# Kernel optimization log

Hardware: AMD Instinct MI355X
Metric: run time of the kernel (lower is better)

The kernel has to match this reference:

```python
import jax, jax.numpy as jnp
import numpy as np

EPS = 1e-08
LAMBDA_SIM = 1.0
LAMBDA_SPARSITY = 0.001
B, D, K = 8192, 4096, 64


def setup_inputs() -> dict:
    key = jax.random.key(0)
    k1, k2, k3, k4, k5 = jax.random.split(key, 5)
    labels = jax.random.randint(k1, (B,), 0, K)
    hard_class_probs = jax.nn.one_hot(labels, K, dtype=jnp.float32)  # [B,K] hard one-hot
    return {
        "hard_class_probs": hard_class_probs,
        "masked_activations_1b": jax.random.normal(k2, (B, D), dtype=jnp.float32),
        "masked_activations_8b": jax.random.normal(k3, (B, D), dtype=jnp.float32),
        "mask_1b": jax.random.uniform(k4, (B, D), dtype=jnp.float32),
        "mask_8b": jax.random.uniform(k5, (B, D), dtype=jnp.float32),
    }


def _classwise_pairwise_cossim(acts, hard_class_probs):
    # F.normalize(p=2, dim=-1, eps=EPS): x / max(||x||, eps)
    norms = jnp.sqrt(jnp.sum(acts * acts, axis=-1, keepdims=True))
    norm_acts = acts / jnp.maximum(norms, EPS)                      # [B,D]
    S = norm_acts @ norm_acts.T                                      # [B,B] gram of unit vectors
    diag = jnp.sum(norm_acts * norm_acts, axis=-1)                   # [B] (== diag(S))
    M = (hard_class_probs > 0.5).astype(acts.dtype)                  # [B,K] hard membership
    n = jnp.sum(M, axis=0)                                           # [K] class counts
    SM = S @ M                                                       # [B,K]
    mSm = jnp.sum(M * SM, axis=0)                                    # [K] sum_{i,j in class} S_ij
    sum_diag = M.T @ diag                                            # [K]
    pair_sum = 0.5 * (mSm - sum_diag)                                # sum over i<j pairs
    n_pairs = 0.5 * n * (n - 1.0)
    valid = n >= 2.0
    per_class_mean = jnp.where(valid, pair_sum / jnp.maximum(n_pairs, 1.0), 0.0)
    n_valid = jnp.sum(valid.astype(acts.dtype))
    return jnp.where(n_valid > 0, jnp.sum(per_class_mean) / jnp.maximum(n_valid, 1.0), 0.0)


def _binary_entropy(p):
    p = jnp.clip(p, EPS, 1.0 - EPS)
    return jnp.mean(-(p * jnp.log(p) + (1.0 - p) * jnp.log(1.0 - p)))


def _combined_loss(hard_class_probs, masked_activations, mask):
    sim_loss = -_classwise_pairwise_cossim(masked_activations, hard_class_probs)
    sparsity_loss = _binary_entropy(mask)
    total = LAMBDA_SIM * sim_loss + LAMBDA_SPARSITY * sparsity_loss
    return total, sim_loss, sparsity_loss


def reference(hard_class_probs, masked_activations_1b, masked_activations_8b, mask_1b, mask_8b):
    loss_1b, sim_1b, sp_1b = _combined_loss(hard_class_probs, masked_activations_1b, mask_1b)
    loss_8b, sim_8b, sp_8b = _combined_loss(hard_class_probs, masked_activations_8b, mask_8b)
    total_loss = loss_1b + loss_8b
    return (total_loss, sim_1b, sim_8b, sp_1b, sp_8b)
```

## Files before the change

kernel.cpp:

```cpp
#include <hip/hip_runtime.h>
#include <math.h>

#define B_ 8192
#define D_ 4096
#define K_ 64
#define EPSF 1e-8f
#define LN2F 0.69314718056f
#define SPLITS 16
#define ECHUNKS 1024

typedef float f32x4 __attribute__((ext_vector_type(4)));


__global__ void k_init(int* __restrict__ z) {
  if (threadIdx.x < 192) z[threadIdx.x] = 0;
}

__global__ void k_labels(const float* __restrict__ probs, int* __restrict__ counts,
                         int* __restrict__ rowlist) {
  int row = blockIdx.x * 4 + (threadIdx.x >> 6);
  int lane = threadIdx.x & 63;
  float p = probs[(size_t)row * K_ + lane];
  unsigned long long m = __ballot(p > 0.5f);
  if (lane == 0) {
    int k = __ffsll(m) - 1;
    if (k >= 0) {
      int pos = atomicAdd(&counts[k], 1);
      rowlist[k * B_ + pos] = row;
    }
  }
}

__device__ __forceinline__ float ent1(float p) {
  p = fminf(fmaxf(p, EPSF), 1.0f - EPSF);
  float q = 1.0f - p;
  float lp = __builtin_amdgcn_logf(p);
  float lq = __builtin_amdgcn_logf(fmaxf(q, 1e-38f));
  return -(p * lp + q * lq);
}

__device__ __forceinline__ float ent4(f32x4 v) {
  return ent1(v.x) + ent1(v.y) + ent1(v.z) + ent1(v.w);
}

__global__ __launch_bounds__(256) void k_fused(
    const float* __restrict__ a1, const float* __restrict__ a8,
    const f32x4* __restrict__ m1, const f32x4* __restrict__ m8,
    const int* __restrict__ counts, const int* __restrict__ rowlist,
    float* __restrict__ Cpart1, float* __restrict__ Cpart8, float* __restrict__ sd1,
    float* __restrict__ sd8, double* __restrict__ entpart) {
  __shared__ float sh[8];
  int t = threadIdx.x;
  if (blockIdx.x & 1) {
    int blk = blockIdx.x >> 1;
    const f32x4* base = ((blk < ECHUNKS) ? m1 : m8) + (size_t)(blk & (ECHUNKS - 1)) * 8192;
    double* ep = entpart + ((blk < ECHUNKS) ? 0 : ECHUNKS);
    float s = 0.f;
#pragma unroll
    for (int o = 0; o < 4; ++o) {
      f32x4 v[8];
#pragma unroll
      for (int j = 0; j < 8; ++j) v[j] = base[t + (o * 8 + j) * 256];
#pragma unroll
      for (int j = 0; j < 8; ++j) s += ent4(v[j]);
    }
#pragma unroll
    for (int o = 32; o > 0; o >>= 1) s += __shfl_down(s, o);
    if ((t & 63) == 0) sh[t >> 6] = s;
    __syncthreads();
    if (t == 0) ep[blk & (ECHUNKS - 1)] = (double)((sh[0] + sh[1] + sh[2] + sh[3]) * LN2F);
  } else {
    int bid2 = blockIdx.x >> 1;
    const float* a = (bid2 < 1024) ? a1 : a8;
    float* Cpart = (bid2 < 1024) ? Cpart1 : Cpart8;
    float* sd = (bid2 < 1024) ? sd1 : sd8;
    int b2 = bid2 & 1023;
    int k = b2 & 63;
    int split = b2 >> 6;
    int wave = t >> 6;
    int lane = t & 63;
    int cnt = counts[k];
    int beg = (cnt * split) / SPLITS;
    int end = (cnt * (split + 1)) / SPLITS;
    const int* rl = rowlist + k * B_;

    f32x4 acc0 = 0.f, acc1 = 0.f, acc2 = 0.f, acc3 = 0.f;
    float sdacc = 0.f;
    int par = 0;
    for (int r = beg; r < end; ++r, par ^= 1) {
      int row = rl[r];
      const f32x4* rp = (const f32x4*)(a + (size_t)row * D_) + (wave * 256 + lane);
      f32x4 v0 = rp[0];
      f32x4 v1 = rp[64];
      f32x4 v2 = rp[128];
      f32x4 v3 = rp[192];
      float s = v0.x * v0.x + v0.y * v0.y + v0.z * v0.z + v0.w * v0.w;
      s += v1.x * v1.x + v1.y * v1.y + v1.z * v1.z + v1.w * v1.w;
      s += v2.x * v2.x + v2.y * v2.y + v2.z * v2.z + v2.w * v2.w;
      s += v3.x * v3.x + v3.y * v3.y + v3.z * v3.z + v3.w * v3.w;
#pragma unroll
      for (int o = 32; o > 0; o >>= 1) s += __shfl_xor(s, o);
      if (lane == 0) sh[par * 4 + wave] = s;
      __syncthreads();
      float stot = sh[par * 4] + sh[par * 4 + 1] + sh[par * 4 + 2] + sh[par * 4 + 3];
      float w = 1.0f / fmaxf(sqrtf(stot), EPSF);
      acc0 += w * v0;
      acc1 += w * v1;
      acc2 += w * v2;
      acc3 += w * v3;
      sdacc += stot * w * w;
    }

    float* cp = Cpart + ((size_t)split * K_ + k) * D_ + wave * 1024;
    *(f32x4*)(cp + 4 * lane) = acc0;
    *(f32x4*)(cp + 4 * (64 + lane)) = acc1;
    *(f32x4*)(cp + 4 * (128 + lane)) = acc2;
    *(f32x4*)(cp + 4 * (192 + lane)) = acc3;
    if (t == 0 && sdacc != 0.f) atomicAdd(&sd[k], sdacc);
  }
}

__global__ __launch_bounds__(256) void k_msm(const float* __restrict__ Cpart1,
                                             const float* __restrict__ Cpart8,
                                             float* __restrict__ msp1,
                                             float* __restrict__ msp8) {
  __shared__ float lds[4];
  int b = blockIdx.x;
  const float* Cpart = (b < 256) ? Cpart1 : Cpart8;
  float* msp = (b < 256) ? msp1 : msp8;
  b &= 255;
  int k = b >> 2;
  int q = b & 3;
  int t = threadIdx.x;
  int col = q * 1024 + 4 * t;
  f32x4 c = 0.f;
#pragma unroll
  for (int s = 0; s < SPLITS; ++s)
    c += *(const f32x4*)(Cpart + ((size_t)s * K_ + k) * D_ + col);
  float sq = c.x * c.x + c.y * c.y + c.z * c.z + c.w * c.w;
#pragma unroll
  for (int o = 32; o > 0; o >>= 1) sq += __shfl_down(sq, o);
  if ((t & 63) == 0) lds[t >> 6] = sq;
  __syncthreads();
  if (t == 0) msp[blockIdx.x & 255] = lds[0] + lds[1] + lds[2] + lds[3];
}

__global__ void k_final(const double* __restrict__ entpart, const int* __restrict__ counts,
                        const float* __restrict__ sd1, const float* __restrict__ sd8,
                        const float* __restrict__ msp1, const float* __restrict__ msp8,
                        float* __restrict__ out) {
  __shared__ double dl[8];
  int t = threadIdx.x;
  double e1 = 0.0, e8 = 0.0;
  for (int i = t; i < ECHUNKS; i += 256) {
    e1 += entpart[i];
    e8 += entpart[ECHUNKS + i];
  }
#pragma unroll
  for (int o = 32; o > 0; o >>= 1) {
    e1 += __shfl_down(e1, o);
    e8 += __shfl_down(e8, o);
  }
  int wid = t >> 6;
  if ((t & 63) == 0) { dl[wid] = e1; dl[4 + wid] = e8; }
  __syncthreads();
  float pcm1 = 0.f, pcm8 = 0.f, valid = 0.f;
  if (t < K_) {
    float mSm1 = msp1[t * 4] + msp1[t * 4 + 1] + msp1[t * 4 + 2] + msp1[t * 4 + 3];
    float mSm8 = msp8[t * 4] + msp8[t * 4 + 1] + msp8[t * 4 + 2] + msp8[t * 4 + 3];
    float n = (float)counts[t];
    bool v = (n >= 2.0f);
    float np = fmaxf(0.5f * n * (n - 1.0f), 1.0f);
    valid = v ? 1.0f : 0.f;
    pcm1 = v ? 0.5f * (mSm1 - sd1[t]) / np : 0.f;
    pcm8 = v ? 0.5f * (mSm8 - sd8[t]) / np : 0.f;
  }
#pragma unroll
  for (int o = 32; o > 0; o >>= 1) {
    pcm1 += __shfl_down(pcm1, o);
    pcm8 += __shfl_down(pcm8, o);
    valid += __shfl_down(valid, o);
  }
  if (t == 0) {
    double etot1 = dl[0] + dl[1] + dl[2] + dl[3];
    double etot8 = dl[4] + dl[5] + dl[6] + dl[7];
    float sp1 = (float)(etot1 / (double)((long long)B_ * D_));
    float sp8 = (float)(etot8 / (double)((long long)B_ * D_));
    float cs1 = (valid > 0.f) ? pcm1 / fmaxf(valid, 1.0f) : 0.f;
    float cs8 = (valid > 0.f) ? pcm8 / fmaxf(valid, 1.0f) : 0.f;
    float sim1 = -cs1, sim8 = -cs8;
    out[0] = sim1 + sim8 + 0.001f * (sp1 + sp8);
    out[1] = sim1;
    out[2] = sim8;
    out[3] = sp1;
    out[4] = sp8;
  }
}


extern "C" void kernel_launch(void* const* d_in, const int* in_sizes, int n_in,
                              void* d_out, int out_size, void* d_ws, size_t ws_size,
                              hipStream_t stream) {
  const float* probs = (const float*)d_in[0];
  const float* a1 = (const float*)d_in[1];
  const float* a8 = (const float*)d_in[2];
  const float* m1 = (const float*)d_in[3];
  const float* m8 = (const float*)d_in[4];
  float* out = (float*)d_out;
  char* ws = (char*)d_ws;

  double* entpart = (double*)(ws + 0);
  int* counts = (int*)(ws + 16384);
  float* sd1 = (float*)(ws + 16640);
  float* sd8 = (float*)(ws + 16896);
  float* msp1 = (float*)(ws + 17152);
  float* msp8 = (float*)(ws + 18176);
  int* rowlist = (int*)(ws + 32768);
  float* Cpart1 = (float*)(ws + 2129920);
  float* Cpart8 = (float*)(ws + 18907136);

  k_init<<<1, 256, 0, stream>>>(counts);
  k_labels<<<B_ / 4, 256, 0, stream>>>(probs, counts, rowlist);
  k_fused<<<4096, 256, 0, stream>>>(a1, a8, (const f32x4*)m1, (const f32x4*)m8, counts,
                                    rowlist, Cpart1, Cpart8, sd1, sd8, entpart);
  k_msm<<<512, 256, 0, stream>>>(Cpart1, Cpart8, msp1, msp8);
  k_final<<<1, 256, 0, stream>>>(entpart, counts, sd1, sd8, msp1, msp8, out);
}
```

Measured before the change: 169.6 us.

## Interleave entropy mask chunks into class-sum blocks within one loop

Before, even and odd blocks did different jobs: odd blocks computed mask entropy and even blocks did the per-class normalized row sums. Now each block does both, mixing its 8 entropy iterations of 4 loads each into the row-sum loop. The grid is halved to 2048 blocks. The aim is to overlap the mask-entropy loads with the latency-bound row-gather loop and cut the number of blocks, at the cost of more registers per thread and an extra barrier and reduction at the end of each block.

```diff
diff --git a/kernel.cpp b/kernel.cpp
--- a/kernel.cpp
+++ b/kernel.cpp
@@ -7,7 +7,7 @@
 #define EPSF 1e-8f
 #define LN2F 0.69314718056f
 #define SPLITS 16
-#define ECHUNKS 1024
+#define ECH 1024
 
 typedef float f32x4 __attribute__((ext_vector_type(4)));
 
@@ -50,50 +50,51 @@
     float* __restrict__ Cpart1, float* __restrict__ Cpart8, float* __restrict__ sd1,
     float* __restrict__ sd8, double* __restrict__ entpart) {
   __shared__ float sh[8];
+  int b = blockIdx.x;
+  int tensor = b >> 10;
+  int g = b & 1023;
+  const float* a = tensor ? a8 : a1;
+  const f32x4* mask = tensor ? m8 : m1;
+  float* Cpart = tensor ? Cpart8 : Cpart1;
+  float* sd = tensor ? sd8 : sd1;
+  double* ep = entpart + tensor * ECH;
+  int k = g & 63;
+  int split = g >> 6;
   int t = threadIdx.x;
-  if (blockIdx.x & 1) {
-    int blk = blockIdx.x >> 1;
-    const f32x4* base = ((blk < ECHUNKS) ? m1 : m8) + (size_t)(blk & (ECHUNKS - 1)) * 8192;
-    double* ep = entpart + ((blk < ECHUNKS) ? 0 : ECHUNKS);
-    float s = 0.f;
-#pragma unroll
-    for (int o = 0; o < 4; ++o) {
-      f32x4 v[8];
-#pragma unroll
-      for (int j = 0; j < 8; ++j) v[j] = base[t + (o * 8 + j) * 256];
-#pragma unroll
-      for (int j = 0; j < 8; ++j) s += ent4(v[j]);
-    }
-#pragma unroll
-    for (int o = 32; o > 0; o >>= 1) s += __shfl_down(s, o);
-    if ((t & 63) == 0) sh[t >> 6] = s;
-    __syncthreads();
-    if (t == 0) ep[blk & (ECHUNKS - 1)] = (double)((sh[0] + sh[1] + sh[2] + sh[3]) * LN2F);
-  } else {
-    int bid2 = blockIdx.x >> 1;
-    const float* a = (bid2 < 1024) ? a1 : a8;
-    float* Cpart = (bid2 < 1024) ? Cpart1 : Cpart8;
-    float* sd = (bid2 < 1024) ? sd1 : sd8;
-    int b2 = bid2 & 1023;
-    int k = b2 & 63;
-    int split = b2 >> 6;
-    int wave = t >> 6;
-    int lane = t & 63;
-    int cnt = counts[k];
-    int beg = (cnt * split) / SPLITS;
-    int end = (cnt * (split + 1)) / SPLITS;
-    const int* rl = rowlist + k * B_;
-
-    f32x4 acc0 = 0.f, acc1 = 0.f, acc2 = 0.f, acc3 = 0.f;
-    float sdacc = 0.f;
-    int par = 0;
-    for (int r = beg; r < end; ++r, par ^= 1) {
-      int row = rl[r];
+  int wave = t >> 6;
+  int lane = t & 63;
+  int cnt = counts[k];
+  int beg = (cnt * split) / SPLITS;
+  int end = (cnt * (split + 1)) / SPLITS;
+  const int* rl = rowlist + k * B_;
+  const f32x4* mbase = mask + (size_t)g * 8192;
+
+  f32x4 acc0 = 0.f, acc1 = 0.f, acc2 = 0.f, acc3 = 0.f;
+  float sdacc = 0.f, entacc = 0.f;
+  int nrows = end - beg;
+  int iters = (nrows > 8) ? nrows : 8;
+  int par = 0;
+  for (int i = 0; i < iters; ++i, par ^= 1) {
+    bool doEnt = (i < 8);
+    bool doRow = (i < nrows);
+    f32x4 e0, e1, e2, e3;
+    if (doEnt) {
+      e0 = mbase[t + (4 * i + 0) * 256];
+      e1 = mbase[t + (4 * i + 1) * 256];
+      e2 = mbase[t + (4 * i + 2) * 256];
+      e3 = mbase[t + (4 * i + 3) * 256];
+    }
+    f32x4 v0, v1, v2, v3;
+    if (doRow) {
+      int row = rl[beg + i];
       const f32x4* rp = (const f32x4*)(a + (size_t)row * D_) + (wave * 256 + lane);
-      f32x4 v0 = rp[0];
-      f32x4 v1 = rp[64];
-      f32x4 v2 = rp[128];
-      f32x4 v3 = rp[192];
+      v0 = rp[0];
+      v1 = rp[64];
+      v2 = rp[128];
+      v3 = rp[192];
+    }
+    if (doEnt) entacc += ent4(e0) + ent4(e1) + ent4(e2) + ent4(e3);
+    if (doRow) {
       float s = v0.x * v0.x + v0.y * v0.y + v0.z * v0.z + v0.w * v0.w;
       s += v1.x * v1.x + v1.y * v1.y + v1.z * v1.z + v1.w * v1.w;
       s += v2.x * v2.x + v2.y * v2.y + v2.z * v2.z + v2.w * v2.w;
@@ -108,16 +109,23 @@
       acc1 += w * v1;
       acc2 += w * v2;
       acc3 += w * v3;
-      sdacc += stot * w * w;
-    }
-
-    float* cp = Cpart + ((size_t)split * K_ + k) * D_ + wave * 1024;
-    *(f32x4*)(cp + 4 * lane) = acc0;
-    *(f32x4*)(cp + 4 * (64 + lane)) = acc1;
-    *(f32x4*)(cp + 4 * (128 + lane)) = acc2;
-    *(f32x4*)(cp + 4 * (192 + lane)) = acc3;
-    if (t == 0 && sdacc != 0.f) atomicAdd(&sd[k], sdacc);
-  }
+      if (t == 0) sdacc += stot * w * w;
+    }
+  }
+
+  float* cp = Cpart + ((size_t)split * K_ + k) * D_ + wave * 1024;
+  *(f32x4*)(cp + 4 * lane) = acc0;
+  *(f32x4*)(cp + 4 * (64 + lane)) = acc1;
+  *(f32x4*)(cp + 4 * (128 + lane)) = acc2;
+  *(f32x4*)(cp + 4 * (192 + lane)) = acc3;
+  if (t == 0 && sdacc != 0.f) atomicAdd(&sd[k], sdacc);
+
+  __syncthreads();
+#pragma unroll
+  for (int o = 32; o > 0; o >>= 1) entacc += __shfl_down(entacc, o);
+  if (lane == 0) sh[wave] = entacc;
+  __syncthreads();
+  if (t == 0) ep[g] = (double)((sh[0] + sh[1] + sh[2] + sh[3]) * LN2F);
 }
 
 __global__ __launch_bounds__(256) void k_msm(const float* __restrict__ Cpart1,
@@ -152,9 +160,9 @@
   __shared__ double dl[8];
   int t = threadIdx.x;
   double e1 = 0.0, e8 = 0.0;
-  for (int i = t; i < ECHUNKS; i += 256) {
+  for (int i = t; i < ECH; i += 256) {
     e1 += entpart[i];
-    e8 += entpart[ECHUNKS + i];
+    e8 += entpart[ECH + i];
   }
 #pragma unroll
   for (int o = 32; o > 0; o >>= 1) {
@@ -221,7 +229,7 @@
 
   k_init<<<1, 256, 0, stream>>>(counts);
   k_labels<<<B_ / 4, 256, 0, stream>>>(probs, counts, rowlist);
-  k_fused<<<4096, 256, 0, stream>>>(a1, a8, (const f32x4*)m1, (const f32x4*)m8, counts,
+  k_fused<<<2048, 256, 0, stream>>>(a1, a8, (const f32x4*)m1, (const f32x4*)m8, counts,
                                     rowlist, Cpart1, Cpart8, sd1, sd8, entpart);
   k_msm<<<512, 256, 0, stream>>>(Cpart1, Cpart8, msp1, msp8);
   k_final<<<1, 256, 0, stream>>>(entpart, counts, sd1, sd8, msp1, msp8, out);
```

After: 171.6 us. No clear change (+1.2%).

## Software-pipeline row loads and group fused-kernel blocks by type in chunks of eight

Applied to the files above, without the earlier changes.

The class-accumulation loop now double-buffers rows: it loads the next row's four vectors before reducing and normalising the current one, so global-load latency overlaps the barrier and reduction. Block-to-work mapping also changes from alternating odd/even blocks to groups of eight consecutive blocks per work type, which changes how entropy and accumulation blocks interleave across the GPU. The prefetch raises register pressure, and the loop body is duplicated through macros.

```diff
diff --git a/kernel.cpp b/kernel.cpp
--- a/kernel.cpp
+++ b/kernel.cpp
@@ -7,7 +7,7 @@
 #define EPSF 1e-8f
 #define LN2F 0.69314718056f
 #define SPLITS 16
-#define ECHUNKS 1024
+#define ECH 1024
 
 typedef float f32x4 __attribute__((ext_vector_type(4)));
 
@@ -50,17 +50,22 @@
     float* __restrict__ Cpart1, float* __restrict__ Cpart8, float* __restrict__ sd1,
     float* __restrict__ sd8, double* __restrict__ entpart) {
   __shared__ float sh[8];
+  int b = blockIdx.x;
+  int grp = b >> 3;
+  int lane8 = b & 7;
+  int type = grp & 1;
+  int id = (grp >> 1) * 8 + lane8;
   int t = threadIdx.x;
-  if (blockIdx.x & 1) {
-    int blk = blockIdx.x >> 1;
-    const f32x4* base = ((blk < ECHUNKS) ? m1 : m8) + (size_t)(blk & (ECHUNKS - 1)) * 8192;
-    double* ep = entpart + ((blk < ECHUNKS) ? 0 : ECHUNKS);
+
+  if (type) {
+    const f32x4* mbase = ((id >> 10) ? m8 : m1) + (size_t)(id & 1023) * 8192;
+    double* ep = entpart + ((id >> 10) ? ECH : 0);
     float s = 0.f;
 #pragma unroll
     for (int o = 0; o < 4; ++o) {
       f32x4 v[8];
 #pragma unroll
-      for (int j = 0; j < 8; ++j) v[j] = base[t + (o * 8 + j) * 256];
+      for (int j = 0; j < 8; ++j) v[j] = mbase[t + (o * 8 + j) * 256];
 #pragma unroll
       for (int j = 0; j < 8; ++j) s += ent4(v[j]);
     }
@@ -68,15 +73,14 @@
     for (int o = 32; o > 0; o >>= 1) s += __shfl_down(s, o);
     if ((t & 63) == 0) sh[t >> 6] = s;
     __syncthreads();
-    if (t == 0) ep[blk & (ECHUNKS - 1)] = (double)((sh[0] + sh[1] + sh[2] + sh[3]) * LN2F);
+    if (t == 0) ep[id & 1023] = (double)((sh[0] + sh[1] + sh[2] + sh[3]) * LN2F);
   } else {
-    int bid2 = blockIdx.x >> 1;
-    const float* a = (bid2 < 1024) ? a1 : a8;
-    float* Cpart = (bid2 < 1024) ? Cpart1 : Cpart8;
-    float* sd = (bid2 < 1024) ? sd1 : sd8;
-    int b2 = bid2 & 1023;
-    int k = b2 & 63;
-    int split = b2 >> 6;
+    int tensor = id >> 10;
+    const float* a = tensor ? a8 : a1;
+    float* Cpart = tensor ? Cpart8 : Cpart1;
+    float* sd = tensor ? sd8 : sd1;
+    int k = id & 63;
+    int split = (id & 1023) >> 6;
     int wave = t >> 6;
     int lane = t & 63;
     int cnt = counts[k];
@@ -86,30 +90,51 @@
 
     f32x4 acc0 = 0.f, acc1 = 0.f, acc2 = 0.f, acc3 = 0.f;
     float sdacc = 0.f;
-    int par = 0;
-    for (int r = beg; r < end; ++r, par ^= 1) {
-      int row = rl[r];
-      const f32x4* rp = (const f32x4*)(a + (size_t)row * D_) + (wave * 256 + lane);
-      f32x4 v0 = rp[0];
-      f32x4 v1 = rp[64];
-      f32x4 v2 = rp[128];
-      f32x4 v3 = rp[192];
-      float s = v0.x * v0.x + v0.y * v0.y + v0.z * v0.z + v0.w * v0.w;
-      s += v1.x * v1.x + v1.y * v1.y + v1.z * v1.z + v1.w * v1.w;
-      s += v2.x * v2.x + v2.y * v2.y + v2.z * v2.z + v2.w * v2.w;
-      s += v3.x * v3.x + v3.y * v3.y + v3.z * v3.z + v3.w * v3.w;
-#pragma unroll
-      for (int o = 32; o > 0; o >>= 1) s += __shfl_xor(s, o);
-      if (lane == 0) sh[par * 4 + wave] = s;
-      __syncthreads();
-      float stot = sh[par * 4] + sh[par * 4 + 1] + sh[par * 4 + 2] + sh[par * 4 + 3];
-      float w = 1.0f / fmaxf(sqrtf(stot), EPSF);
-      acc0 += w * v0;
-      acc1 += w * v1;
-      acc2 += w * v2;
-      acc3 += w * v3;
-      sdacc += stot * w * w;
-    }
+    int nrows = end - beg;
+    f32x4 va0, va1, va2, va3, vb0, vb1, vb2, vb3;
+    int qoff = wave * 256 + lane;
+
+#define LROW(X0, X1, X2, X3, RIDX)                                        \
+    {                                                                     \
+      const f32x4* rp_ = (const f32x4*)(a + (size_t)rl[RIDX] * D_) + qoff;\
+      X0 = rp_[0];                                                        \
+      X1 = rp_[64];                                                       \
+      X2 = rp_[128];                                                      \
+      X3 = rp_[192];                                                      \
+    }
+#define CROW(X0, X1, X2, X3, PAR)                                         \
+    {                                                                     \
+      float s_ = X0.x * X0.x + X0.y * X0.y + X0.z * X0.z + X0.w * X0.w;   \
+      s_ += X1.x * X1.x + X1.y * X1.y + X1.z * X1.z + X1.w * X1.w;        \
+      s_ += X2.x * X2.x + X2.y * X2.y + X2.z * X2.z + X2.w * X2.w;        \
+      s_ += X3.x * X3.x + X3.y * X3.y + X3.z * X3.z + X3.w * X3.w;        \
+      _Pragma("unroll") for (int o = 32; o > 0; o >>= 1)                  \
+          s_ += __shfl_xor(s_, o);                                        \
+      if (lane == 0) sh[(PAR)*4 + wave] = s_;                             \
+      __syncthreads();                                                    \
+      float st_ = sh[(PAR)*4] + sh[(PAR)*4 + 1] + sh[(PAR)*4 + 2] +       \
+                  sh[(PAR)*4 + 3];                                        \
+      float w_ = 1.0f / fmaxf(sqrtf(st_), EPSF);                          \
+      acc0 += w_ * X0;                                                    \
+      acc1 += w_ * X1;                                                    \
+      acc2 += w_ * X2;                                                    \
+      acc3 += w_ * X3;                                                    \
+      if (t == 0) sdacc += st_ * w_ * w_;                                 \
+    }
+
+    if (nrows > 0) {
+      LROW(va0, va1, va2, va3, beg)
+      int i = 0;
+      for (; i + 2 <= nrows; i += 2) {
+        LROW(vb0, vb1, vb2, vb3, beg + i + 1)
+        CROW(va0, va1, va2, va3, 0)
+        if (i + 2 < nrows) LROW(va0, va1, va2, va3, beg + i + 2)
+        CROW(vb0, vb1, vb2, vb3, 1)
+      }
+      if (i < nrows) CROW(va0, va1, va2, va3, 0)
+    }
+#undef LROW
+#undef CROW
 
     float* cp = Cpart + ((size_t)split * K_ + k) * D_ + wave * 1024;
     *(f32x4*)(cp + 4 * lane) = acc0;
@@ -152,9 +177,9 @@
   __shared__ double dl[8];
   int t = threadIdx.x;
   double e1 = 0.0, e8 = 0.0;
-  for (int i = t; i < ECHUNKS; i += 256) {
+  for (int i = t; i < ECH; i += 256) {
     e1 += entpart[i];
-    e8 += entpart[ECHUNKS + i];
+    e8 += entpart[ECH + i];
   }
 #pragma unroll
   for (int o = 32; o > 0; o >>= 1) {
```

Result: no change. 169.6 us (-0.0%).
